# Optimization experiments

Measured on AMD Instinct MI355X. Metric: run time of the kernel, lower is better.

The kernel has to match this reference:

```python
import jax, jax.numpy as jnp
import numpy as np

H = 8          # query heads
HKV = 4        # kv heads
D = 256        # head dim
GROUPS = H // HKV
HIDDEN = 2304
WINDOW = 2048  # sliding window
SOFTCAP = 50.0
SCALE = (HIDDEN // H) ** -0.5  # query_pre_attn_scalar uses hidden//heads, not head_dim
NEG = -1e9
ROPE_BASE = 10000.0


def _rope_tables(L, offset=0, dtype=jnp.float32):
    inv_freq = 1.0 / (ROPE_BASE ** (jnp.arange(0, D, 2, dtype=jnp.float32) / D))
    t = jnp.arange(offset, offset + L, dtype=jnp.float32)
    freqs = jnp.outer(t, inv_freq)                    # [L, D/2]
    emb = jnp.concatenate([freqs, freqs], axis=-1)    # [L, D]
    return jnp.cos(emb).astype(dtype), jnp.sin(emb).astype(dtype)


def _rotate_half(x):
    x1, x2 = jnp.split(x, 2, axis=-1)
    return jnp.concatenate([-x2, x1], axis=-1)


def _apply_rope(x, cos, sin):
    # x: [B, h, L, D]; cos/sin: [L, D]
    return x * cos[None, None] + _rotate_half(x) * sin[None, None]


def setup_inputs() -> dict:
    key = jax.random.key(0)
    ks = jax.random.split(key, 5)
    B, L = 1, 4096
    x = jax.random.normal(ks[0], (B, L, HIDDEN), dtype=jnp.float32)
    wq = jax.random.normal(ks[1], (HIDDEN, H * D), dtype=jnp.float32) * 0.02
    wk = jax.random.normal(ks[2], (HIDDEN, HKV * D), dtype=jnp.float32) * 0.02
    wv = jax.random.normal(ks[3], (HIDDEN, HKV * D), dtype=jnp.float32) * 0.02
    wo = jax.random.normal(ks[4], (H * D, HIDDEN), dtype=jnp.float32) * 0.02
    # additive causal mask [1,1,L,L]
    causal = jnp.triu(jnp.full((L, L), NEG, dtype=jnp.float32), k=1)
    mask = causal[None, None]
    return {"x": x, "mask": mask, "wq": wq, "wk": wk, "wv": wv, "wo": wo}


def reference(x, mask, wq, wk, wv, wo):
    B, L, _ = x.shape
    q = (x @ wq).reshape(B, L, H, D).transpose(0, 2, 1, 3)     # [B,H,L,D]
    k = (x @ wk).reshape(B, L, HKV, D).transpose(0, 2, 1, 3)   # [B,HKV,L,D]
    v = (x @ wv).reshape(B, L, HKV, D).transpose(0, 2, 1, 3)

    cos, sin = _rope_tables(L, 0, q.dtype)
    q = _apply_rope(q, cos, sin)
    k = _apply_rope(k, cos, sin)

    # GQA: repeat_interleave kv heads
    k = jnp.repeat(k, GROUPS, axis=1)  # [B,H,L,D]
    v = jnp.repeat(v, GROUPS, axis=1)

    attn = jnp.einsum("bhqd,bhkd->bhqk", q, k) * SCALE
    attn = SOFTCAP * jnp.tanh(attn / SOFTCAP)
    attn = attn + mask

    kv_len = attn.shape[-1]
    if kv_len > WINDOW:  # sliding branch: keep only last WINDOW key columns
        col_keep = jnp.arange(kv_len) >= (kv_len - WINDOW)  # [kv_len]
        attn = jnp.where(col_keep[None, None, None, :], attn, NEG)

    attn = jax.nn.softmax(attn.astype(jnp.float32), axis=-1).astype(q.dtype)
    out = jnp.einsum("bhqk,bhkd->bhqd", attn, v)
    out = out.transpose(0, 2, 1, 3).reshape(B, L, H * D)
    return out @ wo
```

## Files before the change

kernel.cpp:

```cpp
#include <hip/hip_runtime.h>

typedef unsigned short u16;
typedef __bf16 bf16x8 __attribute__((ext_vector_type(8)));
typedef float floatx4 __attribute__((ext_vector_type(4)));
typedef unsigned short u16x4 __attribute__((ext_vector_type(4)));
typedef unsigned short u16x8 __attribute__((ext_vector_type(8)));

#define L_SEQ 4096
#define HID   2304
#define NH    8
#define NKV   4
#define HD    256
#define QDIM  2048
#define KVDIM 1024
#define SCALE_F 0.05892556509887896f

__device__ __forceinline__ u16 f2bf(float f) {
  unsigned u = __float_as_uint(f);
  u += 0x7FFFu + ((u >> 16) & 1u);
  return (u16)(u >> 16);
}
__device__ __forceinline__ float bf2f(u16 h) {
  return __uint_as_float(((unsigned)h) << 16);
}

__device__ __forceinline__ void async_load16(const u16* g, u16* lds_base) {
  __builtin_amdgcn_global_load_lds(
      (const __attribute__((address_space(1))) unsigned int*)g,
      (__attribute__((address_space(3))) unsigned int*)lds_base, 16, 0, 0);
}

__device__ __forceinline__ int swz(int m) { return (m + (m >> 2)) & 3; }

__global__ __launch_bounds__(256)
void cast_kernel(const float* __restrict__ in, u16* __restrict__ out, int n4) {
  int i = blockIdx.x * 256 + threadIdx.x;
  if (i < n4) {
    float4 v = *reinterpret_cast<const float4*>(&in[(size_t)i * 4]);
    u16x4 o;
    o[0] = f2bf(v.x); o[1] = f2bf(v.y); o[2] = f2bf(v.z); o[3] = f2bf(v.w);
    *reinterpret_cast<u16x4*>(&out[(size_t)i * 4]) = o;
  }
}

__global__ __launch_bounds__(256)
void transpose_kernel(const float* __restrict__ wq, const float* __restrict__ wk,
                      const float* __restrict__ wv, const float* __restrict__ wo,
                      u16* __restrict__ wqkvT, u16* __restrict__ woT) {
  const int z = blockIdx.z;
  const float* W; u16* WT; int K, N;
  if (z == 0)      { W = wq; WT = wqkvT;                            K = HID;  N = QDIM; }
  else if (z == 1) { W = wk; WT = wqkvT + (size_t)QDIM * HID;       K = HID;  N = KVDIM; }
  else if (z == 2) { W = wv; WT = wqkvT + (size_t)(QDIM + KVDIM) * HID; K = HID; N = KVDIM; }
  else             { W = wo; WT = woT;                              K = QDIM; N = HID; }
  const int n0 = blockIdx.x * 32, k0 = blockIdx.y * 32;
  if (n0 >= N || k0 >= K) return;
  __shared__ u16 t[32][33];
  const int c = threadIdx.x & 31, r4 = (threadIdx.x >> 5) * 4;
#pragma unroll
  for (int i = 0; i < 4; ++i)
    t[r4 + i][c] = f2bf(W[(size_t)(k0 + r4 + i) * N + n0 + c]);
  __syncthreads();
  const int nn = threadIdx.x & 31, kb = (threadIdx.x >> 5) * 4;
  u16x4 o;
#pragma unroll
  for (int j = 0; j < 4; ++j) o[j] = t[kb + j][nn];
  *reinterpret_cast<u16x4*>(&WT[(size_t)(n0 + nn) * K + k0 + kb]) = o;
}

#define G256_NT 36

#define G256_BARRIER() __builtin_amdgcn_s_barrier()
#define G256_SCHEDB()  __builtin_amdgcn_sched_barrier(0)

#define G256_STAGE(bb, X, kh, tt)                                              \
  {                                                                            \
    const u16* g = (X) ? BT + (size_t)(n0 + w * 32 + srow) * HID               \
                       : A + (size_t)(m0 + w * 32 + srow) * HID;               \
    const int kc = (tt) * 64 + (kh) * 32 + schk;                               \
    async_load16(g + kc, &lds[bb][X][kh][(w * 32) * 32]);                      \
    async_load16(g + 16 * HID + kc, &lds[bb][X][kh][(w * 32 + 16) * 32]);      \
  }

#define G256_RD_B(dst, bb, kk)                                                 \
  {                                                                            \
    const u16* Bk = &lds[bb][1][kk][0];                                        \
    _Pragma("unroll") for (int nt = 0; nt < 4; ++nt)                           \
        dst[nt] = *reinterpret_cast<const bf16x8*>(                            \
            &Bk[(wn + nt * 16 + l16) * 32 + rsw]);                             \
  }

#define G256_RD_A(dst, bb, kk, ch)                                             \
  {                                                                            \
    const u16* Ak = &lds[bb][0][kk][0];                                        \
    _Pragma("unroll") for (int mt = 0; mt < 4; ++mt)                           \
        dst[mt] = *reinterpret_cast<const bf16x8*>(                            \
            &Ak[(wm + ((ch) * 4 + mt) * 16 + l16) * 32 + rsw]);                \
  }

#define G256_MFMA(ch, AA, BB)                                                  \
  {                                                                            \
    __builtin_amdgcn_s_setprio(1);                                             \
    _Pragma("unroll") for (int mt = 0; mt < 4; ++mt)                           \
        _Pragma("unroll") for (int nt = 0; nt < 4; ++nt)                       \
            acc[(ch) * 4 + mt][nt] = __builtin_amdgcn_mfma_f32_16x16x32_bf16(  \
                AA[mt], BB[nt], acc[(ch) * 4 + mt][nt], 0, 0, 0);              \
    __builtin_amdgcn_s_setprio(0);                                             \
  }

#define G256_VMCNT4() __asm__ volatile("s_waitcnt vmcnt(4)")
#define G256_VMCNT0() __asm__ volatile("s_waitcnt vmcnt(0)")

__global__ __launch_bounds__(512)
void gemm256_kernel(const u16* __restrict__ A, const u16* __restrict__ BT,
                    u16* __restrict__ C) {
  __shared__ __align__(16) u16 lds[2][2][2][256 * 32];

  const int tid  = threadIdx.x;
  const int lane = tid & 63;
  const int w    = tid >> 6;
  const int l16  = lane & 15;
  const int quad = lane >> 4;
  const int wm   = (w >> 2) * 128;
  const int wn   = (w & 3) * 64;

  const int srow = lane >> 2;
  const int schk = (((lane & 3) ^ ((lane >> 3) & 3))) * 8;
  const int rsw = ((quad ^ ((l16 >> 1) & 3))) * 8;

  const int bid = blockIdx.x;
  const int id  = (bid & 7) * 20 + (bid >> 3);

  int m0, n0, region;
  if (id < 64)      { region = 0; n0 = (id & 7) * 256;          m0 = 2048 + (id >> 3) * 256; }
  else if (id < 96) { region = 1; const int i = id - 64;
                      n0 = 2048 + (i & 3) * 256;                m0 = 2048 + (i >> 2) * 256; }
  else              { region = 2; const int i = id - 96;
                      n0 = 3072 + (i & 3) * 256;                m0 = (i >> 2) * 256; }

  floatx4 acc[8][4];
#pragma unroll
  for (int i = 0; i < 8; ++i)
#pragma unroll
    for (int j = 0; j < 4; ++j) acc[i][j] = (floatx4){0.f, 0.f, 0.f, 0.f};

  G256_STAGE(0, 0, 0, 0); G256_STAGE(0, 1, 0, 0);
  G256_STAGE(0, 0, 1, 0); G256_STAGE(0, 1, 1, 0);
  G256_STAGE(1, 0, 0, 1); G256_STAGE(1, 1, 0, 1);
  G256_VMCNT4();
  G256_BARRIER();

#pragma unroll 2
  for (int t = 0; t < G256_NT; ++t) {
    const int bb = t & 1;
    bf16x8 a_cur[4], b_cur[4], a_hi0[4], a_lo1[4], b1[4], a_hi1[4];

    G256_RD_A(a_cur, bb, 0, 0);
    G256_RD_B(b_cur, bb, 0);
    G256_RD_A(a_hi0, bb, 0, 1);
    if (t + 1 < G256_NT) { G256_STAGE(bb ^ 1, 0, 1, t + 1); }
    G256_SCHEDB();
    G256_MFMA(0, a_cur, b_cur);
    G256_BARRIER();

    G256_RD_A(a_lo1, bb, 1, 0);
    G256_RD_B(b1, bb, 1);
    if (t + 1 < G256_NT) { G256_STAGE(bb ^ 1, 1, 1, t + 1); }
    G256_SCHEDB();
    G256_MFMA(1, a_hi0, b_cur);
    G256_BARRIER();

    G256_RD_A(a_hi1, bb, 1, 1);
    if (t + 2 < G256_NT) { G256_STAGE(bb, 0, 0, t + 2); }
    G256_SCHEDB();
    G256_MFMA(0, a_lo1, b1);
    G256_BARRIER();

    if (t + 2 < G256_NT) { G256_STAGE(bb, 1, 0, t + 2); }
    G256_SCHEDB();
    G256_MFMA(1, a_hi1, b1);
    if (t < G256_NT - 2) { G256_VMCNT4(); }
    else                 { G256_VMCNT0(); }
    G256_BARRIER();
  }

#pragma unroll
  for (int mt = 0; mt < 8; ++mt)
#pragma unroll
    for (int nt = 0; nt < 4; ++nt) {
      const int mbase = m0 + wm + mt * 16 + quad * 4;
      const int n = n0 + wn + nt * 16 + l16;
      if (region == 0) {
        const size_t base = (size_t)(n >> 8) * L_SEQ * HD + (n & 255);
#pragma unroll
        for (int r = 0; r < 4; ++r)
          C[base + (size_t)(mbase + r) * HD] = f2bf(acc[mt][nt][r] * SCALE_F);
      } else if (region == 1) {
        const int nk2 = n - QDIM;
        const size_t base = (size_t)NH * L_SEQ * HD +
                            (size_t)(nk2 >> 8) * L_SEQ * HD + (nk2 & 255);
#pragma unroll
        for (int r = 0; r < 4; ++r)
          C[base + (size_t)(mbase + r) * HD] = f2bf(acc[mt][nt][r]);
      } else {
        const int nv = n - QDIM - KVDIM;
        u16x4 o;
#pragma unroll
        for (int r = 0; r < 4; ++r) o[r] = f2bf(acc[mt][nt][r]);
        *reinterpret_cast<u16x4*>(
            &C[(size_t)(NH + NKV) * L_SEQ * HD +
               ((size_t)(nv >> 8) * HD + (nv & 255)) * L_SEQ + mbase]) = o;
      }
    }
}

template<int MODE>
__global__ __launch_bounds__(256)
void gemm_kernel(const u16* __restrict__ A, const u16* __restrict__ BT,
                 void* __restrict__ Cp, int N, int K) {
  __shared__ __align__(16) u16 Alds[128][32];
  __shared__ __align__(16) u16 Blds[128][32];

  const int tid  = threadIdx.x;
  const int lane = tid & 63;
  const int w    = tid >> 6;
  const int wm   = (w >> 1) * 64;
  const int wn   = (w & 1) * 64;
  const int l16  = lane & 15;
  const int quad = lane >> 4;

  int m0, n0;
  if (MODE == 0) {
    const int id = blockIdx.x;
    if (id < 256)      { n0 = (id & 15) * 128;                 m0 = 2048 + (id >> 4) * 128; }
    else if (id < 384) { const int i2 = id - 256;
                         n0 = 2048 + (i2 & 7) * 128;           m0 = 2048 + (i2 >> 3) * 128; }
    else               { const int i3 = id - 384;
                         n0 = 3072 + (i3 & 7) * 128;           m0 = (i3 >> 3) * 128; }
  } else {
    m0 = blockIdx.y * 128;
    n0 = blockIdx.x * 128;
  }

  const int srow_in = lane >> 2;
  const int schunk  = lane & 3;

  floatx4 acc[4][4];
#pragma unroll
  for (int i = 0; i < 4; ++i)
#pragma unroll
    for (int j = 0; j < 4; ++j) acc[i][j] = (floatx4){0.f, 0.f, 0.f, 0.f};

  const int nk = K >> 5;
  for (int kt = 0; kt < nk; ++kt) {
    __syncthreads();
#pragma unroll
    for (int p = 0; p < 2; ++p) {
      const int row = w * 32 + p * 16 + srow_in;
      const int ce  = schunk ^ swz(row);
      async_load16(&A[(size_t)(m0 + row) * K + kt * 32 + ce * 8], &Alds[w * 32 + p * 16][0]);
      async_load16(&BT[(size_t)(n0 + row) * K + kt * 32 + ce * 8], &Blds[w * 32 + p * 16][0]);
    }
    __syncthreads();

    bf16x8 a[4], b[4];
#pragma unroll
    for (int mt = 0; mt < 4; ++mt) {
      const int row = wm + mt * 16 + l16;
      a[mt] = *reinterpret_cast<const bf16x8*>(&Alds[row][(quad ^ swz(row)) * 8]);
    }
#pragma unroll
    for (int nt = 0; nt < 4; ++nt) {
      const int row = wn + nt * 16 + l16;
      b[nt] = *reinterpret_cast<const bf16x8*>(&Blds[row][(quad ^ swz(row)) * 8]);
    }
#pragma unroll
    for (int mt = 0; mt < 4; ++mt)
#pragma unroll
      for (int nt = 0; nt < 4; ++nt)
        acc[mt][nt] = __builtin_amdgcn_mfma_f32_16x16x32_bf16(a[mt], b[nt], acc[mt][nt], 0, 0, 0);
  }

#pragma unroll
  for (int mt = 0; mt < 4; ++mt)
#pragma unroll
    for (int nt = 0; nt < 4; ++nt) {
      const int mbase = m0 + wm + mt * 16 + quad * 4;
      const int n = n0 + wn + nt * 16 + l16;
      if (MODE == 0) {
        u16* C = (u16*)Cp;
        if (n < QDIM) {
          const size_t base = (size_t)(n >> 8) * L_SEQ * HD + (n & 255);
#pragma unroll
          for (int r = 0; r < 4; ++r)
            C[base + (size_t)(mbase + r) * HD] = f2bf(acc[mt][nt][r]);
        } else if (n < QDIM + KVDIM) {
          const int nk2 = n - QDIM;
          const size_t base = (size_t)NH * L_SEQ * HD +
                              (size_t)(nk2 >> 8) * L_SEQ * HD + (nk2 & 255);
#pragma unroll
          for (int r = 0; r < 4; ++r)
            C[base + (size_t)(mbase + r) * HD] = f2bf(acc[mt][nt][r]);
        } else {
          const int nv = n - QDIM - KVDIM;
          u16x4 o;
#pragma unroll
          for (int r = 0; r < 4; ++r) o[r] = f2bf(acc[mt][nt][r]);
          *reinterpret_cast<u16x4*>(
              &C[(size_t)(NH + NKV) * L_SEQ * HD +
                 ((size_t)(nv >> 8) * HD + (nv & 255)) * L_SEQ + mbase]) = o;
        }
      } else {
        float* C = (float*)Cp;
#pragma unroll
        for (int r = 0; r < 4; ++r)
          C[(size_t)(mbase + r) * N + n] = acc[mt][nt][r];
      }
    }
}

__global__ __launch_bounds__(128)
void rope_kernel(u16* __restrict__ qb, u16* __restrict__ kb) {
  const int l  = 2048 + blockIdx.x;
  const int hh = blockIdx.y;
  u16* base = (hh < NH) ? qb + ((size_t)hh * L_SEQ + l) * HD
                        : kb + ((size_t)(hh - NH) * L_SEQ + l) * HD;
  const int d = threadIdx.x;
  const float invf = exp2f((float)d * (-13.287712379549449f / 128.0f));
  const float ang = (float)l * invf;
  float s, c;
  sincosf(ang, &s, &c);
  const float x1 = bf2f(base[d]);
  const float x2 = bf2f(base[d + 128]);
  base[d]       = f2bf(x1 * c - x2 * s);
  base[d + 128] = f2bf(x2 * c + x1 * s);
}

__global__ __launch_bounds__(256)
void meanv_kernel(const u16* __restrict__ vt, float* __restrict__ mv) {
  const int row  = blockIdx.x * 4 + (threadIdx.x >> 6);
  const int lane = threadIdx.x & 63;
  const u16* p = vt + (size_t)row * L_SEQ;
  float s = 0.f;
#pragma unroll
  for (int c = 0; c < 8; ++c) {
    u16x8 v = *reinterpret_cast<const u16x8*>(&p[(c * 64 + lane) * 8]);
#pragma unroll
    for (int j = 0; j < 8; ++j) s += bf2f(v[j]);
  }
#pragma unroll
  for (int off = 32; off > 0; off >>= 1) s += __shfl_xor(s, off, 64);
  if (lane == 0) mv[row] = s * (1.0f / 4096.0f);
}

__global__ __launch_bounds__(256)
void rowvec_part_kernel(const float* __restrict__ mv, const float* __restrict__ wo,
                        float* __restrict__ rpart) {
  const int j = blockIdx.x * 256 + threadIdx.x;
  const int c0 = blockIdx.y * 128;
  float acc = 0.f;
#pragma unroll 4
  for (int cc = 0; cc < 128; ++cc) {
    const int c = c0 + cc;
    const float a = mv[((c >> 9) << 8) | (c & 255)];
    acc += a * wo[(size_t)c * HID + j];
  }
  rpart[blockIdx.y * HID + j] = acc;
}

__global__ __launch_bounds__(256)
void rowvec_reduce_kernel(const float* __restrict__ rpart, float* __restrict__ r) {
  const int j = blockIdx.x * 256 + threadIdx.x;
  float s = 0.f;
#pragma unroll
  for (int p = 0; p < 16; ++p) s += rpart[p * HID + j];
  r[j] = s;
}

__global__ __launch_bounds__(256)
void bcast_out_kernel(const float* __restrict__ r, float* __restrict__ out) {
  const int idx = blockIdx.x * 256 + threadIdx.x;
  const int col4 = idx % 576;
  *reinterpret_cast<float4*>(&out[(size_t)idx * 4]) =
      *reinterpret_cast<const float4*>(&r[col4 * 4]);
}

#define ATT_STAGE(g_, buf_)                                                    \
  {                                                                            \
    const int kt_ = r_off[run] + (g_);                                         \
    const u16* kg_ = kg0 + (size_t)kt_ * 32 * HD;                              \
    _Pragma("unroll") for (int p_ = 0; p_ < 4; ++p_) {                         \
      const int r_   = w * 8 + p_ * 2 + (lane >> 5);                           \
      const int pos_ = lane & 31;                                              \
      const int c_   = (pos_ & 24) | ((pos_ ^ r_) & 7);                        \
      async_load16(&kg_[(size_t)r_ * HD + c_ * 8],                             \
                   &Klds[buf_][(w * 8 + p_ * 2) * 256]);                       \
    }                                                                          \
    const u16* vg_ = vg0 + kt_ * 32;                                           \
    _Pragma("unroll") for (int j_ = 0; j_ < 4; ++j_) {                         \
      const int m_  = w * 32 + j_ * 8 + (lane >> 3);                           \
      const int p2_ = lane & 7;                                                \
      const int c2_ = p2_ ^ (m_ & 7);                                          \
      const int r2_ = m_ * 2 + (c2_ >> 2);                                     \
      async_load16(&vg_[(size_t)r2_ * L_SEQ + (c2_ & 3) * 8],                  \
                   &Vlds[buf_][(w * 32 + j_ * 8) * 64]);                       \
    }                                                                          \
  }

__global__ __launch_bounds__(256)
void attn_kernel(const u16* __restrict__ qb, const u16* __restrict__ kb,
                 const u16* __restrict__ vt, u16* __restrict__ Opart,
                 float* __restrict__ lpart) {
  const int s = blockIdx.x;
  const int pr = blockIdx.y;
  const int h = blockIdx.z;
  const int kvh = h >> 1;
  const int tid = threadIdx.x;
  const int w = tid >> 6, lane = tid & 63;
  const int l16 = lane & 15, quad = lane >> 4;

  __shared__ __align__(16) u16 Klds[2][32 * 256];
  __shared__ __align__(16) u16 Vlds[2][256 * 32];
  __shared__ u16 Plds[4][16][40];

  const int n_a = 2 * pr + 2;
  const int lo = (66 * s) >> 2;
  const int hi = (66 * (s + 1)) >> 2;

  const int r_lo[2] = {lo, (lo > n_a) ? lo : n_a};
  const int r_hi[2] = {(hi < n_a) ? hi : n_a, hi};
  const int r_t[2]  = {32 + pr, 63 - pr};
  const int r_off[2] = {64, 64 - n_a};

  const u16* kg0 = kb + (size_t)kvh * L_SEQ * HD;
  const u16* vg0 = vt + (size_t)kvh * HD * L_SEQ;

  for (int run = 0; run < 2; ++run) {
    if (r_lo[run] >= r_hi[run]) continue;
    const int t  = r_t[run];
    const int q0 = t * 64 + w * 16;
    const int glo = r_lo[run], ghi = r_hi[run];

    bf16x8 aq[8];
    {
      const u16* qr = qb + ((size_t)h * L_SEQ + q0 + l16) * HD + quad * 8;
#pragma unroll
      for (int f = 0; f < 8; ++f)
        aq[f] = *reinterpret_cast<const bf16x8*>(&qr[f * 32]);
#pragma unroll
      for (int f = 0; f < 8; ++f) {
        floatx4& t4 = reinterpret_cast<floatx4&>(aq[f]);
        __asm__ volatile("" : "+v"(t4));
      }
    }

    ATT_STAGE(glo, 0);
    if (glo + 1 < ghi) ATT_STAGE(glo + 1, 1);

    floatx4 acc[16];
#pragma unroll
    for (int i = 0; i < 16; ++i) acc[i] = (floatx4){0.f, 0.f, 0.f, 0.f};
    float lsum[4] = {0.f, 0.f, 0.f, 0.f};

    for (int g = glo; g < ghi; ++g) {
      const int cur = (g - glo) & 1;
      const int kt = r_off[run] + g;
      if (g + 1 < ghi) { __asm__ volatile("s_waitcnt vmcnt(8)"); }
      else             { __asm__ volatile("s_waitcnt vmcnt(0)"); }
      __builtin_amdgcn_s_barrier();

      const u16* Kb = &Klds[cur][0];
      const u16* Vb = &Vlds[cur][0];

      floatx4 sa[2] = {(floatx4){0.f, 0.f, 0.f, 0.f}, (floatx4){0.f, 0.f, 0.f, 0.f}};
#pragma unroll
      for (int nt = 0; nt < 2; ++nt) {
        const int row = nt * 16 + l16;
#pragma unroll
        for (int f = 0; f < 8; ++f) {
          const int c   = f * 4 + quad;
          const int pos = (c & 24) | ((c ^ row) & 7);
          bf16x8 bk = *reinterpret_cast<const bf16x8*>(&Kb[row * 256 + pos * 8]);
          sa[nt] = __builtin_amdgcn_mfma_f32_16x16x32_bf16(aq[f], bk, sa[nt], 0, 0, 0);
        }
      }
#pragma unroll
      for (int nt = 0; nt < 2; ++nt) {
        const int key = kt * 32 + nt * 16 + l16;
#pragma unroll
        for (int r = 0; r < 4; ++r) {
          const float x = sa[nt][r];
          const float capm50 = -100.0f / (__expf(x * 0.04f) + 1.0f);
          float p = __expf(capm50);
          const int qq = q0 + quad * 4 + r;
          p = (key <= qq) ? p : 0.0f;
          lsum[r] += p;
          Plds[w][quad * 4 + r][nt * 16 + l16] = f2bf(p);
        }
      }
      bf16x8 ap = *reinterpret_cast<const bf16x8*>(&Plds[w][l16][quad * 8]);
#pragma unroll
      for (int dt = 0; dt < 16; ++dt) {
        const int rV = dt * 16 + l16;
        const int m  = rV >> 1;
        const int p  = ((rV & 1) * 4 + quad) ^ (m & 7);
        bf16x8 bv = *reinterpret_cast<const bf16x8*>(&Vb[m * 64 + p * 8]);
        acc[dt] = __builtin_amdgcn_mfma_f32_16x16x32_bf16(ap, bv, acc[dt], 0, 0, 0);
      }

      __builtin_amdgcn_s_barrier();
      if (g + 2 < ghi) ATT_STAGE(g + 2, cur);
    }

#pragma unroll
    for (int r = 0; r < 4; ++r) {
      float l = lsum[r];
      l += __shfl_xor(l, 1); l += __shfl_xor(l, 2);
      l += __shfl_xor(l, 4); l += __shfl_xor(l, 8);
      lsum[r] = l;
    }
    const int ql0 = q0 - 2048 + quad * 4;
#pragma unroll
    for (int r = 0; r < 4; ++r) {
      u16* orow = Opart + (((size_t)s * NH + h) * 2048 + ql0 + r) * HD + l16;
#pragma unroll
      for (int dt = 0; dt < 16; ++dt) orow[dt * 16] = f2bf(acc[dt][r]);
      if (l16 == 0) lpart[((size_t)s * NH + h) * 2048 + ql0 + r] = lsum[r];
    }
  }
}

__global__ __launch_bounds__(256)
void combine_kernel(const u16* __restrict__ Opart, const float* __restrict__ lpart,
                    u16* __restrict__ ab) {
  const int idx4 = blockIdx.x * 256 + threadIdx.x;
  const int d4 = (idx4 & 63) * 4;
  const int ql = (idx4 >> 6) & 2047;
  const int h  = idx4 >> 17;
  const int qtile = ql >> 6;
  const bool role_a = qtile < 16;
  const int pr = role_a ? qtile : 31 - qtile;
  const int lo_s[4] = {0, 16, 33, 49};
  const int hi_s[4] = {16, 33, 49, 66};

  float4 o = {0.f, 0.f, 0.f, 0.f};
  float l = 0.f;
#pragma unroll
  for (int s = 0; s < 4; ++s) {
    const bool valid = role_a ? (lo_s[s] < 2 * pr + 2) : (hi_s[s] > 2 * pr + 2);
    if (valid) {
      u16x4 v = *reinterpret_cast<const u16x4*>(
          &Opart[(((size_t)s * NH + h) * 2048 + ql) * HD + d4]);
      o.x += bf2f(v[0]); o.y += bf2f(v[1]); o.z += bf2f(v[2]); o.w += bf2f(v[3]);
      l += lpart[((size_t)s * NH + h) * 2048 + ql];
    }
  }
  const float inv = 1.0f / l;
  u16x4 ov;
  ov[0] = f2bf(o.x * inv); ov[1] = f2bf(o.y * inv);
  ov[2] = f2bf(o.z * inv); ov[3] = f2bf(o.w * inv);
  *reinterpret_cast<u16x4*>(&ab[(size_t)(2048 + ql) * QDIM + h * HD + d4]) = ov;
}

extern "C" void kernel_launch(void* const* d_in, const int* in_sizes, int n_in,
                              void* d_out, int out_size, void* d_ws, size_t ws_size,
                              hipStream_t stream) {
  const float* x  = (const float*)d_in[0];
  const float* wq = (const float*)d_in[2];
  const float* wk = (const float*)d_in[3];
  const float* wv = (const float*)d_in[4];
  const float* wo = (const float*)d_in[5];
  float* out = (float*)d_out;

  u16* qb  = (u16*)d_ws;
  u16* kb  = qb  + (size_t)NH  * L_SEQ * HD;
  u16* vtb = kb  + (size_t)NKV * L_SEQ * HD;
  u16* ab  = vtb + (size_t)NKV * L_SEQ * HD;
  u16* xb  = ab  + (size_t)L_SEQ * QDIM;
  u16* wqkvT = xb + (size_t)L_SEQ * HID;
  u16* woT = wqkvT + (size_t)(QDIM + 2 * KVDIM) * HID;
  u16* Opart = woT + (size_t)HID * QDIM;
  float* lpart = (float*)(Opart + (size_t)4 * NH * 2048 * HD);
  float* mv    = lpart + (size_t)4 * NH * 2048;
  float* rpart = mv + 1024;
  float* rvec  = rpart + 16 * HID;

  cast_kernel<<<dim3(L_SEQ * HID / 4 / 256), 256, 0, stream>>>(x, xb, L_SEQ * HID / 4);
  transpose_kernel<<<dim3(72, 72, 4), 256, 0, stream>>>(wq, wk, wv, wo, wqkvT, woT);

  gemm256_kernel<<<dim3(160), 512, 0, stream>>>(xb, wqkvT, qb);
  rope_kernel<<<dim3(L_SEQ / 2, NH + NKV), 128, 0, stream>>>(qb, kb);
  meanv_kernel<<<dim3(256), 256, 0, stream>>>(vtb, mv);

  rowvec_part_kernel<<<dim3(9, 16), 256, 0, stream>>>(mv, wo, rpart);
  rowvec_reduce_kernel<<<dim3(9), 256, 0, stream>>>(rpart, rvec);
  bcast_out_kernel<<<dim3(2048 * 576 / 256), 256, 0, stream>>>(rvec, out);

  attn_kernel<<<dim3(4, 16, NH), 256, 0, stream>>>(qb, kb, vtb, Opart, lpart);
  combine_kernel<<<dim3(4096), 256, 0, stream>>>(Opart, lpart, ab);

  gemm_kernel<1><<<dim3(HID / 128, 2048 / 128), 256, 0, stream>>>(
      ab + (size_t)2048 * QDIM, woT, out + (size_t)2048 * HID, HID, QDIM);
}
```

Baseline: 362.6 us.

## Double-buffer output projection GEMM with async LDS prefetch and block swizzle

Replaces the generic single-buffered output GEMM with a specialized kernel. It uses double-buffered LDS staging split into two K-halves, prefetches the next tile while the MFMAs run, raises wave priority around the MFMA blocks, and remaps block IDs for better L2 locality. The aim is to hide global-load latency that the old sync-load-compute loop exposed. In exchange it uses twice the LDS and hardcodes the problem shape.

Result: faster. 339.9 us (-6.3%).

```diff
diff --git a/kernel.cpp b/kernel.cpp
--- a/kernel.cpp
+++ b/kernel.cpp
@@ -29,8 +29,6 @@
       (const __attribute__((address_space(1))) unsigned int*)g,
       (__attribute__((address_space(3))) unsigned int*)lds_base, 16, 0, 0);
 }
-
-__device__ __forceinline__ int swz(int m) { return (m + (m >> 2)) & 3; }
 
 __global__ __launch_bounds__(256)
 void cast_kernel(const float* __restrict__ in, u16* __restrict__ out, int n4) {
@@ -214,36 +212,60 @@
     }
 }
 
-template<int MODE>
-__global__ __launch_bounds__(256)
-void gemm_kernel(const u16* __restrict__ A, const u16* __restrict__ BT,
-                 void* __restrict__ Cp, int N, int K) {
-  __shared__ __align__(16) u16 Alds[128][32];
-  __shared__ __align__(16) u16 Blds[128][32];
+#define GOUT_NT 32
+
+#define GOUT_STAGE(bb, X, kh, tt)                                              \
+  {                                                                            \
+    const u16* g = (X) ? BT + (size_t)(n0 + w * 32 + srow) * QDIM              \
+                       : A + (size_t)(m0 + w * 32 + srow) * QDIM;              \
+    const int kc = (tt) * 64 + (kh) * 32 + schk;                               \
+    async_load16(g + kc, &lds[bb][X][kh][(w * 32) * 32]);                      \
+    async_load16(g + 16 * QDIM + kc, &lds[bb][X][kh][(w * 32 + 16) * 32]);     \
+  }
+
+#define GOUT_RD(dstA, dstB, bb, kk)                                            \
+  {                                                                            \
+    const u16* Ak = &lds[bb][0][kk][0];                                        \
+    const u16* Bk = &lds[bb][1][kk][0];                                        \
+    _Pragma("unroll") for (int mt = 0; mt < 4; ++mt)                           \
+        dstA[mt] = *reinterpret_cast<const bf16x8*>(                           \
+            &Ak[(wm + mt * 16 + l16) * 32 + rsw]);                             \
+    _Pragma("unroll") for (int nt = 0; nt < 4; ++nt)                           \
+        dstB[nt] = *reinterpret_cast<const bf16x8*>(                           \
+            &Bk[(wn + nt * 16 + l16) * 32 + rsw]);                             \
+  }
+
+#define GOUT_MFMA(AA, BB)                                                      \
+  {                                                                            \
+    __builtin_amdgcn_s_setprio(1);                                             \
+    _Pragma("unroll") for (int mt = 0; mt < 4; ++mt)                           \
+        _Pragma("unroll") for (int nt = 0; nt < 4; ++nt)                       \
+            acc[mt][nt] = __builtin_amdgcn_mfma_f32_16x16x32_bf16(             \
+                AA[mt], BB[nt], acc[mt][nt], 0, 0, 0);                         \
+    __builtin_amdgcn_s_setprio(0);                                             \
+  }
+
+__global__ __launch_bounds__(256)
+void gemm_out_kernel(const u16* __restrict__ A, const u16* __restrict__ BT,
+                     float* __restrict__ C) {
+  __shared__ __align__(16) u16 lds[2][2][2][128 * 32];
 
   const int tid  = threadIdx.x;
   const int lane = tid & 63;
   const int w    = tid >> 6;
+  const int l16  = lane & 15;
+  const int quad = lane >> 4;
   const int wm   = (w >> 1) * 64;
   const int wn   = (w & 1) * 64;
-  const int l16  = lane & 15;
-  const int quad = lane >> 4;
-
-  int m0, n0;
-  if (MODE == 0) {
-    const int id = blockIdx.x;
-    if (id < 256)      { n0 = (id & 15) * 128;                 m0 = 2048 + (id >> 4) * 128; }
-    else if (id < 384) { const int i2 = id - 256;
-                         n0 = 2048 + (i2 & 7) * 128;           m0 = 2048 + (i2 >> 3) * 128; }
-    else               { const int i3 = id - 384;
-                         n0 = 3072 + (i3 & 7) * 128;           m0 = (i3 >> 3) * 128; }
-  } else {
-    m0 = blockIdx.y * 128;
-    n0 = blockIdx.x * 128;
-  }
-
-  const int srow_in = lane >> 2;
-  const int schunk  = lane & 3;
+
+  const int srow = lane >> 2;
+  const int schk = (((lane & 3) ^ ((lane >> 3) & 3))) * 8;
+  const int rsw  = ((quad ^ ((l16 >> 1) & 3))) * 8;
+
+  const int bid = blockIdx.x;
+  const int id  = (bid & 7) * 36 + (bid >> 3);
+  const int n0  = (id % 18) * 128;
+  const int m0  = (id / 18) * 128;
 
   floatx4 acc[4][4];
 #pragma unroll
@@ -251,34 +273,32 @@
 #pragma unroll
     for (int j = 0; j < 4; ++j) acc[i][j] = (floatx4){0.f, 0.f, 0.f, 0.f};
 
-  const int nk = K >> 5;
-  for (int kt = 0; kt < nk; ++kt) {
-    __syncthreads();
-#pragma unroll
-    for (int p = 0; p < 2; ++p) {
-      const int row = w * 32 + p * 16 + srow_in;
-      const int ce  = schunk ^ swz(row);
-      async_load16(&A[(size_t)(m0 + row) * K + kt * 32 + ce * 8], &Alds[w * 32 + p * 16][0]);
-      async_load16(&BT[(size_t)(n0 + row) * K + kt * 32 + ce * 8], &Blds[w * 32 + p * 16][0]);
-    }
-    __syncthreads();
-
-    bf16x8 a[4], b[4];
-#pragma unroll
-    for (int mt = 0; mt < 4; ++mt) {
-      const int row = wm + mt * 16 + l16;
-      a[mt] = *reinterpret_cast<const bf16x8*>(&Alds[row][(quad ^ swz(row)) * 8]);
-    }
-#pragma unroll
-    for (int nt = 0; nt < 4; ++nt) {
-      const int row = wn + nt * 16 + l16;
-      b[nt] = *reinterpret_cast<const bf16x8*>(&Blds[row][(quad ^ swz(row)) * 8]);
-    }
-#pragma unroll
-    for (int mt = 0; mt < 4; ++mt)
-#pragma unroll
-      for (int nt = 0; nt < 4; ++nt)
-        acc[mt][nt] = __builtin_amdgcn_mfma_f32_16x16x32_bf16(a[mt], b[nt], acc[mt][nt], 0, 0, 0);
+  GOUT_STAGE(0, 0, 0, 0); GOUT_STAGE(0, 1, 0, 0);
+  GOUT_STAGE(0, 0, 1, 0); GOUT_STAGE(0, 1, 1, 0);
+  GOUT_STAGE(1, 0, 0, 1); GOUT_STAGE(1, 1, 0, 1);
+  G256_VMCNT4();
+  G256_BARRIER();
+
+#pragma unroll 2
+  for (int t = 0; t < GOUT_NT; ++t) {
+    const int bb = t & 1;
+    bf16x8 a0[4], b0[4], a1[4], b1[4];
+
+    GOUT_RD(a0, b0, bb, 0);
+    GOUT_RD(a1, b1, bb, 1);
+    if (t + 1 < GOUT_NT) { GOUT_STAGE(bb ^ 1, 0, 1, t + 1);
+                           GOUT_STAGE(bb ^ 1, 1, 1, t + 1); }
+    G256_SCHEDB();
+    GOUT_MFMA(a0, b0);
+    G256_BARRIER();
+
+    if (t + 2 < GOUT_NT) { GOUT_STAGE(bb, 0, 0, t + 2);
+                           GOUT_STAGE(bb, 1, 0, t + 2); }
+    G256_SCHEDB();
+    GOUT_MFMA(a1, b1);
+    if (t < GOUT_NT - 2) { G256_VMCNT4(); }
+    else                 { G256_VMCNT0(); }
+    G256_BARRIER();
   }
 
 #pragma unroll
@@ -287,35 +307,9 @@
     for (int nt = 0; nt < 4; ++nt) {
       const int mbase = m0 + wm + mt * 16 + quad * 4;
       const int n = n0 + wn + nt * 16 + l16;
-      if (MODE == 0) {
-        u16* C = (u16*)Cp;
-        if (n < QDIM) {
-          const size_t base = (size_t)(n >> 8) * L_SEQ * HD + (n & 255);
-#pragma unroll
-          for (int r = 0; r < 4; ++r)
-            C[base + (size_t)(mbase + r) * HD] = f2bf(acc[mt][nt][r]);
-        } else if (n < QDIM + KVDIM) {
-          const int nk2 = n - QDIM;
-          const size_t base = (size_t)NH * L_SEQ * HD +
-                              (size_t)(nk2 >> 8) * L_SEQ * HD + (nk2 & 255);
-#pragma unroll
-          for (int r = 0; r < 4; ++r)
-            C[base + (size_t)(mbase + r) * HD] = f2bf(acc[mt][nt][r]);
-        } else {
-          const int nv = n - QDIM - KVDIM;
-          u16x4 o;
-#pragma unroll
-          for (int r = 0; r < 4; ++r) o[r] = f2bf(acc[mt][nt][r]);
-          *reinterpret_cast<u16x4*>(
-              &C[(size_t)(NH + NKV) * L_SEQ * HD +
-                 ((size_t)(nv >> 8) * HD + (nv & 255)) * L_SEQ + mbase]) = o;
-        }
-      } else {
-        float* C = (float*)Cp;
-#pragma unroll
-        for (int r = 0; r < 4; ++r)
-          C[(size_t)(mbase + r) * N + n] = acc[mt][nt][r];
-      }
+#pragma unroll
+      for (int r = 0; r < 4; ++r)
+        C[(size_t)(mbase + r) * HID + n] = acc[mt][nt][r];
     }
 }
 
@@ -599,6 +593,6 @@
   attn_kernel<<<dim3(4, 16, NH), 256, 0, stream>>>(qb, kb, vtb, Opart, lpart);
   combine_kernel<<<dim3(4096), 256, 0, stream>>>(Opart, lpart, ab);
 
-  gemm_kernel<1><<<dim3(HID / 128, 2048 / 128), 256, 0, stream>>>(
-      ab + (size_t)2048 * QDIM, woT, out + (size_t)2048 * HID, HID, QDIM);
-}
+  gemm_out_kernel<<<dim3(288), 256, 0, stream>>>(
+      ab + (size_t)2048 * QDIM, woT, out + (size_t)2048 * HID);
+}
```
